# Performance work log

Hardware: AMD Instinct MI355X
Metric: run time of the kernel (lower is better)

## Reference

```python
import jax, jax.numpy as jnp
import numpy as np

POS_THR = 0.7
NEG_THR = 0.3
SAMPLE_BATCH = 256
POS_FRAC = 0.5
B, K, H, W, G = 8, 9, 64, 64, 128
A = K * H * W  # 36864 total anchors


def _make_boxes(key, lead_shape, img=1024.0, wmin=16.0, wmax=256.0):
    k1, k2 = jax.random.split(key)
    ctr = jax.random.uniform(k1, lead_shape + (2,), minval=0.0, maxval=img)
    wh = jax.random.uniform(k2, lead_shape + (2,), minval=wmin, maxval=wmax)
    return jnp.concatenate([ctr - wh / 2, ctr + wh / 2], axis=-1)


def setup_inputs() -> dict:
    key = jax.random.key(0)
    k1, k2, k3, k4 = jax.random.split(key, 4)
    return {
        "cls_logits": jax.random.normal(k1, (B, K, H, W), dtype=jnp.float32),
        "bbox_pred": jax.random.normal(k2, (B, 4 * K, H, W), dtype=jnp.float32) * 0.1,
        "anchors": _make_boxes(k3, (A,)),
        "gt_boxes": _make_boxes(k4, (B, G)),
    }


def _compute_iou(a, g):
    # a: [A,4], g: [G,4] -> [A,G]
    lt = jnp.maximum(a[:, None, :2], g[None, :, :2])
    rb = jnp.minimum(a[:, None, 2:], g[None, :, 2:])
    wh = jnp.clip(rb - lt, 0.0)
    inter = wh[..., 0] * wh[..., 1]
    area_a = (a[:, 2] - a[:, 0]) * (a[:, 3] - a[:, 1])
    area_g = (g[:, 2] - g[:, 0]) * (g[:, 3] - g[:, 1])
    return inter / (area_a[:, None] + area_g[None, :] - inter + 1e-6)


def _encode(anchors, gt):
    aw = anchors[:, 2] - anchors[:, 0]
    ah = anchors[:, 3] - anchors[:, 1]
    acx = (anchors[:, 0] + anchors[:, 2]) / 2
    acy = (anchors[:, 1] + anchors[:, 3]) / 2
    gw = gt[:, 2] - gt[:, 0]
    gh = gt[:, 3] - gt[:, 1]
    gcx = (gt[:, 0] + gt[:, 2]) / 2
    gcy = (gt[:, 1] + gt[:, 3]) / 2
    return jnp.stack([(gcx - acx) / aw, (gcy - acy) / ah,
                      jnp.log(gw / aw), jnp.log(gh / ah)], axis=1)


def _subsample(labels, mask, target, key):
    # deterministic-key analog of torch.randperm subsampling: random priorities,
    # keep the `target` highest-priority anchors of the masked class.
    score = jnp.where(mask, jax.random.uniform(key, labels.shape), -1.0)
    order = jnp.argsort(-score)
    rank = jnp.zeros_like(order).at[order].set(jnp.arange(order.shape[0]))
    keep = mask & (rank < target)
    return jnp.where(mask & ~keep, -1, labels)


def _per_image(cls_i, box_i, anchors, gt, key):
    iou = _compute_iou(anchors, gt)                      # [A,G]
    max_iou = iou.max(axis=1)
    matched_gt_idx = iou.argmax(axis=1)
    labels = jnp.where(max_iou < NEG_THR, 0, -1)
    labels = jnp.where(max_iou >= POS_THR, 1, labels)
    matched_anchor_idx = iou.argmax(axis=0)              # [G]
    labels = labels.at[matched_anchor_idx].set(1)        # force best anchor per gt
    bbox_targets = _encode(anchors, gt[matched_gt_idx])  # [A,4]

    k1, k2 = jax.random.split(key)
    pos_mask0 = labels == 1
    num_pos = pos_mask0.sum()
    target_pos = jnp.minimum(jnp.int32(SAMPLE_BATCH * POS_FRAC), num_pos)
    labels = _subsample(labels, pos_mask0, target_pos, k1)
    neg_mask0 = labels == 0
    num_neg = neg_mask0.sum()
    target_neg = jnp.minimum(SAMPLE_BATCH - target_pos, num_neg)
    labels = _subsample(labels, neg_mask0, target_neg, k2)

    valid = (labels >= 0).astype(cls_i.dtype)
    z = (labels == 1).astype(cls_i.dtype)
    # BCEWithLogits: softplus(x) - x*z
    bce = jax.nn.softplus(cls_i) - cls_i * z
    cls_loss = (bce * valid).sum() / jnp.maximum(valid.sum(), 1.0)

    pos = (labels == 1).astype(cls_i.dtype)
    d = box_i - bbox_targets
    ad = jnp.abs(d)
    sl1 = jnp.where(ad < 1.0, 0.5 * d * d, ad - 0.5)     # SmoothL1, beta=1
    bbox_loss = (sl1 * pos[:, None]).sum() / jnp.maximum(4.0 * pos.sum(), 1.0)
    return cls_loss, bbox_loss


def reference(cls_logits, bbox_pred, anchors, gt_boxes):
    b = cls_logits.shape[0]
    cls = cls_logits.transpose(0, 2, 3, 1).reshape(b, -1)          # [B,A]
    box = bbox_pred.transpose(0, 2, 3, 1).reshape(b, -1, 4)        # [B,A,4]
    keys = jax.random.split(jax.random.key(42), b)
    cls_l, box_l = jax.vmap(_per_image, in_axes=(0, 0, None, 0, 0))(
        cls, box, anchors, gt_boxes, keys)
    cls_loss = cls_l.mean()
    bbox_loss = box_l.mean()
    return jnp.stack([cls_loss, bbox_loss, cls_loss + bbox_loss])
```

## Files before the change

### kernel.cpp

```cpp
#include <hip/hip_runtime.h>
#include <stdint.h>
#include <limits.h>

#define PARTITIONABLE 1

#define B_ 8
#define K_ 9
#define H_ 64
#define W_ 64
#define G_ 128
#define A_ 36864
#define HALF_A 18432
#define NBUCK 1024
#define BSHIFT 13
#define CAP 1024
#define NLAB  1152
#define NPB   144

struct KeyParams { uint32_t k[B_][4]; };

__host__ __device__ static inline uint32_t rotl32(uint32_t x, int r) {
  return (x << r) | (x >> (32 - r));
}

__host__ __device__ static inline void tf2x32(uint32_t k0, uint32_t k1,
                                              uint32_t x0, uint32_t x1,
                                              uint32_t& o0, uint32_t& o1) {
  uint32_t ks2 = k0 ^ k1 ^ 0x1BD11BDAu;
  x0 += k0; x1 += k1;
#define TF_R(r) { x0 += x1; x1 = rotl32(x1, r); x1 ^= x0; }
  TF_R(13) TF_R(15) TF_R(26) TF_R(6)
  x0 += k1;  x1 += ks2 + 1u;
  TF_R(17) TF_R(29) TF_R(16) TF_R(24)
  x0 += ks2; x1 += k0 + 2u;
  TF_R(13) TF_R(15) TF_R(26) TF_R(6)
  x0 += k0;  x1 += k1 + 3u;
  TF_R(17) TF_R(29) TF_R(16) TF_R(24)
  x0 += k1;  x1 += ks2 + 4u;
  TF_R(13) TF_R(15) TF_R(26) TF_R(6)
  x0 += ks2; x1 += k0 + 5u;
#undef TF_R
  o0 = x0; o1 = x1;
}

__device__ static inline uint32_t anchor_vbits(uint32_t k0, uint32_t k1, int a) {
  uint32_t o0, o1;
#if PARTITIONABLE
  tf2x32(k0, k1, 0u, (uint32_t)a, o0, o1);
  return (o0 ^ o1) >> 9;
#else
  if (a < HALF_A) { tf2x32(k0, k1, (uint32_t)a, (uint32_t)(a + HALF_A), o0, o1); return o0 >> 9; }
  else            { tf2x32(k0, k1, (uint32_t)(a - HALF_A), (uint32_t)a, o0, o1); return o1 >> 9; }
#endif
}

__device__ static inline float area_of(float x0, float y0, float x1, float y1) {
#pragma clang fp contract(off)
  return (x1 - x0) * (y1 - y0);
}

__device__ static inline float iou_pre_a(float a0, float a1, float a2, float a3,
                                         float area_a,
                                         float g0, float g1, float g2, float g3) {
#pragma clang fp contract(off)
  float ltx = fmaxf(a0, g0), lty = fmaxf(a1, g1);
  float rbx = fminf(a2, g2), rby = fminf(a3, g3);
  float w = rbx - ltx; w = (w < 0.f) ? 0.f : w;
  float h = rby - lty; h = (h < 0.f) ? 0.f : h;
  float inter  = w * h;
  float area_g = (g2 - g0) * (g3 - g1);
  return inter / (area_a + area_g - inter + 1e-6f);
}

__device__ static inline void encode4(float4 an, float4 gg, float* tt) {
#pragma clang fp contract(off)
  float aw  = an.z - an.x,            ah  = an.w - an.y;
  float acx = (an.x + an.z) * 0.5f,   acy = (an.y + an.w) * 0.5f;
  float gw  = gg.z - gg.x,            gh  = gg.w - gg.y;
  float gcx = (gg.x + gg.z) * 0.5f,   gcy = (gg.y + gg.w) * 0.5f;
  tt[0] = (gcx - acx) / aw;
  tt[1] = (gcy - acy) / ah;
  tt[2] = logf(gw / aw);
  tt[3] = logf(gh / ah);
}

__device__ static inline int block_reduce_int(int v, int* sh) {
  int t = threadIdx.x;
  sh[t] = v; __syncthreads();
  for (int s = 128; s > 0; s >>= 1) { if (t < s) sh[t] += sh[t + s]; __syncthreads(); }
  int r = sh[0]; __syncthreads();
  return r;
}
__device__ static inline float block_reduce_float(float v, float* sh) {
  int t = threadIdx.x;
  sh[t] = v; __syncthreads();
  for (int s = 128; s > 0; s >>= 1) { if (t < s) sh[t] += sh[t + s]; __syncthreads(); }
  float r = sh[0]; __syncthreads();
  return r;
}

__device__ static inline void st_agent_i32(int* p, int v) {
  __hip_atomic_store(p, v, __ATOMIC_RELAXED, __HIP_MEMORY_SCOPE_AGENT);
}
__device__ static inline void st_agent_u32(uint32_t* p, uint32_t v) {
  __hip_atomic_store(p, v, __ATOMIC_RELAXED, __HIP_MEMORY_SCOPE_AGENT);
}
__device__ static inline int ld_agent_i32(const int* p) {
  return __hip_atomic_load(p, __ATOMIC_RELAXED, __HIP_MEMORY_SCOPE_AGENT);
}
__device__ static inline uint32_t ld_agent_u32(const uint32_t* p) {
  return __hip_atomic_load(p, __ATOMIC_RELAXED, __HIP_MEMORY_SCOPE_AGENT);
}
__device__ static inline unsigned long long ld_agent_u64(const unsigned long long* p) {
  return __hip_atomic_load(p, __ATOMIC_RELAXED, __HIP_MEMORY_SCOPE_AGENT);
}
__device__ static inline float ld_agent_f32(const float* p) {
  return __hip_atomic_load(p, __ATOMIC_RELAXED, __HIP_MEMORY_SCOPE_AGENT);
}

__global__ __launch_bounds__(256) void iou_k(
    const float* __restrict__ anchors, const float* __restrict__ gtb,
    int* __restrict__ labels, int* __restrict__ mgt,
    uint32_t* __restrict__ vpos, uint32_t* __restrict__ vneg,
    int* __restrict__ ghist, int* __restrict__ counts,
    unsigned long long* __restrict__ gmax,
    int* __restrict__ cbR, int* __restrict__ targets,
    int* __restrict__ tickets, KeyParams kp) {
  __shared__ float2 gp01[2 * G_];
  __shared__ float2 gp23[2 * G_];
  __shared__ unsigned long long slot2[2 * G_];
  __shared__ int red[256];
  __shared__ int sup[16];
  __shared__ int last;

  const int bid = blockIdx.x;
  const int t = threadIdx.x;
  const int b  = bid / NPB;
  const int xb = bid % NPB;
  const int a  = xb * 256 + t;
  const size_t idx = (size_t)b * A_ + a;

  {
    if (t < G_) {
      float4 gg = ((const float4*)gtb)[b * G_ + t];
      float2 p01; p01.x = gg.x; p01.y = gg.y;
      float2 p23; p23.x = gg.z; p23.y = gg.w;
      gp01[t] = p01; gp01[t + G_] = p01;
      gp23[t] = p23; gp23[t + G_] = p23;
    }
    slot2[t] = 0ull;
    __syncthreads();

    float4 an = ((const float4*)anchors)[a];
    float area_a = area_of(an.x, an.y, an.z, an.w);
    const int t7 = t & (G_ - 1);
    const unsigned long long alow = (unsigned long long)(~(uint32_t)a);
    unsigned long long blp = 0ull;
#pragma unroll 4
    for (int s = 0; s < G_; s++) {
      const int gi = t7 + s;
      float2 p01 = gp01[gi];
      float2 p23 = gp23[gi];
      float v = iou_pre_a(an.x, an.y, an.z, an.w, area_a,
                          p01.x, p01.y, p23.x, p23.y);
      unsigned long long hi = (unsigned long long)__float_as_uint(v) << 32;
      unsigned long long lp = hi | (unsigned)((gi & (G_ - 1)) ^ (G_ - 1));
      if (lp > blp) blp = lp;
      atomicMax(&slot2[gi], hi | alow);
    }
    __syncthreads();
    if (t < G_) {
      unsigned long long p = slot2[t];
      unsigned long long q = slot2[t + G_];
      if (q > p) p = q;
      atomicMax(&gmax[b * G_ + t], p);
    }

    float bv = __uint_as_float((uint32_t)(blp >> 32));
    int   bi = ((int)(blp & (unsigned long long)(G_ - 1))) ^ (G_ - 1);
    int lb = (bv < 0.3f) ? 0 : ((bv >= 0.7f) ? 1 : -1);
    uint32_t vp = anchor_vbits(kp.k[b][0], kp.k[b][1], a);
    uint32_t vn = anchor_vbits(kp.k[b][2], kp.k[b][3], a);
    st_agent_i32(&labels[idx], lb);
    st_agent_u32(&vpos[idx], vp);
    st_agent_u32(&vneg[idx], vn);
    mgt[idx] = bi;
    if (lb == 1)      atomicAdd(&ghist[(b * 2 + 0) * NBUCK + (vp >> BSHIFT)], 1);
    else if (lb == 0) atomicAdd(&ghist[(b * 2 + 1) * NBUCK + (vn >> BSHIFT)], 1);
    int packed = (lb == 1 ? 1 : 0) | ((lb == 0 ? 1 : 0) << 16);
    int rr = block_reduce_int(packed, red);
    if (t == 0) {
      atomicAdd(&counts[b * 2 + 0], rr & 0xFFFF);
      atomicAdd(&counts[b * 2 + 1], rr >> 16);
    }
  }

  __syncthreads();
  if (t == 0) {
    int v = __hip_atomic_fetch_add(&tickets[b], 1, __ATOMIC_RELAXED,
                                   __HIP_MEMORY_SCOPE_AGENT);
    last = (v == NPB - 1);
  }
  __syncthreads();
  if (!last) return;

  if (t < G_) {
    unsigned long long gm = ld_agent_u64(&gmax[b * G_ + t]);
    int fa = (int)(~(uint32_t)(gm & 0xFFFFFFFFull));
    size_t fidx = (size_t)b * A_ + fa;
    int old = atomicExch(&labels[fidx], 1);
    if (old != 1) {
      atomicAdd(&counts[b * 2 + 0], 1);
      atomicAdd(&ghist[(b * 2 + 0) * NBUCK + (ld_agent_u32(&vpos[fidx]) >> BSHIFT)], 1);
      if (old == 0) {
        atomicSub(&counts[b * 2 + 1], 1);
        atomicSub(&ghist[(b * 2 + 1) * NBUCK + (ld_agent_u32(&vneg[fidx]) >> BSHIFT)], 1);
      }
    }
  }
  __syncthreads();

  int npos = ld_agent_i32(&counts[b * 2 + 0]);
  int nneg = ld_agent_i32(&counts[b * 2 + 1]);
  int tp = npos < 128 ? npos : 128;
  int tn = 256 - tp; if (nneg < tn) tn = nneg;
  for (int c = 0; c < 2; ++c) {
    const int row = b * 2 + c;
    const int target = (c == 0) ? tp : tn;
    const int* hist = ghist + (size_t)row * NBUCK;
    { int s = 0; const int base = t * 4;
      for (int i = 0; i < 4; i++) s += ld_agent_i32(&hist[base + i]);
      red[t] = s; }
    __syncthreads();
    if (t < 16) { int ss = 0; for (int j = 0; j < 16; j++) ss += red[t * 16 + j]; sup[t] = ss; }
    __syncthreads();
    if (t == 0) {
      int cb = INT_MAX, R = 0;
      if (target > 0) {
        int cum = 0, si = 0;
        for (int i = 15; i >= 0; i--) { if (cum + sup[i] >= target) { si = i; break; } cum += sup[i]; }
        int sj = si * 16;
        for (int j = si * 16 + 15; j >= si * 16; j--) { if (cum + red[j] >= target) { sj = j; break; } cum += red[j]; }
        for (int k = sj * 4 + 3; k >= sj * 4; k--) {
          int hv = ld_agent_i32(&hist[k]);
          if (cum + hv >= target) { cb = k; R = target - cum; break; }
          cum += hv;
        }
      }
      st_agent_i32(&cbR[row * 2 + 0], cb);
      st_agent_i32(&cbR[row * 2 + 1], R);
      st_agent_i32(&targets[row], target);
    }
    __syncthreads();
  }
}

__global__ __launch_bounds__(256) void loss2_k(
    const float* __restrict__ anchors, const float* __restrict__ gtb,
    const float* __restrict__ cls, const float* __restrict__ boxp,
    const int* __restrict__ labels, const int* __restrict__ mgt,
    const uint32_t* __restrict__ vpos, const uint32_t* __restrict__ vneg,
    const int* __restrict__ cbR, const int* __restrict__ targets,
    int* __restrict__ ccnt, uint32_t* __restrict__ cvv, int* __restrict__ cii,
    float* __restrict__ bsums, int* __restrict__ tickets,
    float* __restrict__ out) {
  __shared__ float redf[256];
  __shared__ uint32_t scv[CAP];
  __shared__ int sci[CAP];
  __shared__ int last;

  const int bid = blockIdx.x;
  const int t = threadIdx.x;
  const int b  = bid / NPB;
  const int xb = bid % NPB;
  const int a  = xb * 256 + t;
  const size_t idx = (size_t)b * A_ + a;

  {
    float sb = 0.f, ss = 0.f;
    int lb = labels[idx];
    if (lb >= 0) {
      int c = (lb == 1) ? 0 : 1;
      int row = b * 2 + c;
      uint32_t v = (c == 0 ? vpos : vneg)[idx];
      int bucket = (int)(v >> BSHIFT);
      int cb = cbR[row * 2];
      if (bucket == cb) {
        int p = atomicAdd(&ccnt[row], 1);
        if (p < CAP) {
          st_agent_u32(&cvv[row * CAP + p], v);
          st_agent_i32(&cii[row * CAP + p], a);
        }
      } else if (bucket > cb) {
        int kk = a % K_; int hw = a / K_; int hh = hw / W_; int wx = hw % W_;
        float x  = cls[(((size_t)b * K_ + kk) * H_ + hh) * W_ + wx];
        float sp = fmaxf(x, 0.f) + log1pf(expf(-fabsf(x)));
        sb = (lb == 1) ? (sp - x) : sp;
        if (lb == 1) {
          float4 an = ((const float4*)anchors)[a];
          int    mg = mgt[idx];
          float4 gg = ((const float4*)gtb)[b * G_ + mg];
          float tt[4]; encode4(an, gg, tt);
          for (int cc2 = 0; cc2 < 4; cc2++) {
            float p = boxp[(((size_t)b * (4 * K_) + (4 * kk + cc2)) * H_ + hh) * W_ + wx];
            float d = p - tt[cc2];
            float ad = fabsf(d);
            ss += (ad < 1.f) ? (0.5f * d * d) : (ad - 0.5f);
          }
        }
      }
    }
    float sbT = block_reduce_float(sb, redf);
    float ssT = block_reduce_float(ss, redf);
    if (t == 0) {
      if (sbT != 0.f) atomicAdd(&bsums[b * 2 + 0], sbT);
      if (ssT != 0.f) atomicAdd(&bsums[b * 2 + 1], ssT);
    }
  }

  __syncthreads();
  if (t == 0) {
    int v = __hip_atomic_fetch_add(&tickets[8 + b], 1, __ATOMIC_RELAXED,
                                   __HIP_MEMORY_SCOPE_AGENT);
    last = (v == NPB - 1);
  }
  __syncthreads();
  if (!last) return;

  for (int c = 0; c < 2; ++c) {
    const int row = b * 2 + c;
    int c2 = ld_agent_i32(&ccnt[row]); if (c2 > CAP) c2 = CAP;
    const int R = cbR[row * 2 + 1];
    for (int j = t; j < c2; j += 256) {
      scv[j] = ld_agent_u32(&cvv[row * CAP + j]);
      sci[j] = ld_agent_i32(&cii[row * CAP + j]);
    }
    __syncthreads();
    const bool pos = (c == 0);
    float sbl = 0.f, ssl = 0.f;
    for (int j = t; j < c2; j += 256) {
      uint32_t v = scv[j]; int a2 = sci[j];
      int r = 0;
      for (int k2 = 0; k2 < c2; k2++) {
        uint32_t vk = scv[k2]; int ik = sci[k2];
        if (vk > v || (vk == v && ik < a2)) r++;
      }
      if (r < R) {
        int kk = a2 % K_; int hw = a2 / K_; int hh = hw / W_; int wx = hw % W_;
        float x = cls[(((size_t)b * K_ + kk) * H_ + hh) * W_ + wx];
        float sp = fmaxf(x, 0.f) + log1pf(expf(-fabsf(x)));
        sbl += pos ? (sp - x) : sp;
        if (pos) {
          float4 an = ((const float4*)anchors)[a2];
          int mg = mgt[(size_t)b * A_ + a2];
          float4 gg = ((const float4*)gtb)[b * G_ + mg];
          float tt[4]; encode4(an, gg, tt);
          for (int cc2 = 0; cc2 < 4; cc2++) {
            float p = boxp[(((size_t)b * (4 * K_) + (4 * kk + cc2)) * H_ + hh) * W_ + wx];
            float d = p - tt[cc2];
            float ad = fabsf(d);
            ssl += (ad < 1.f) ? (0.5f * d * d) : (ad - 0.5f);
          }
        }
      }
    }
    float sbT = block_reduce_float(sbl, redf);
    float ssT = block_reduce_float(ssl, redf);
    if (t == 0) {
      if (sbT != 0.f) atomicAdd(&bsums[b * 2 + 0], sbT);
      if (ssT != 0.f) atomicAdd(&bsums[b * 2 + 1], ssT);
    }
    __syncthreads();
  }

  __syncthreads();
  if (t == 0) {
    int v = __hip_atomic_fetch_add(&tickets[16], 1, __ATOMIC_RELAXED,
                                   __HIP_MEMORY_SCOPE_AGENT);
    last = (v == B_ - 1);
  }
  __syncthreads();
  if (!last) return;

  if (t == 0) {
    float cl = 0.f, bl = 0.f;
    for (int bb = 0; bb < B_; bb++) {
      int tpv = ld_agent_i32(&targets[bb * 2 + 0]);
      int tnv = ld_agent_i32(&targets[bb * 2 + 1]);
      float s0 = ld_agent_f32(&bsums[bb * 2 + 0]);
      float s1 = ld_agent_f32(&bsums[bb * 2 + 1]);
      cl += s0 / fmaxf((float)(tpv + tnv), 1.f);
      bl += s1 / fmaxf(4.f * (float)tpv, 1.f);
    }
    cl *= 0.125f; bl *= 0.125f;
    out[0] = cl; out[1] = bl; out[2] = cl + bl;
  }
}

static void compute_keys(KeyParams& kp) {
  const uint32_t r0 = 0u, r1 = 42u;
#if PARTITIONABLE
  for (int b = 0; b < B_; b++) {
    uint32_t kb0, kb1;
    tf2x32(r0, r1, 0u, (uint32_t)b, kb0, kb1);
    uint32_t a0, a1, c0, c1;
    tf2x32(kb0, kb1, 0u, 0u, a0, a1);
    tf2x32(kb0, kb1, 0u, 1u, c0, c1);
    kp.k[b][0] = a0; kp.k[b][1] = a1; kp.k[b][2] = c0; kp.k[b][3] = c1;
  }
#else
  uint32_t o0[8], o1[8], flat[16];
  for (int i = 0; i < 8; i++) tf2x32(r0, r1, (uint32_t)i, (uint32_t)(8 + i), o0[i], o1[i]);
  for (int i = 0; i < 8; i++) { flat[i] = o0[i]; flat[8 + i] = o1[i]; }
  for (int b = 0; b < B_; b++) {
    uint32_t kb0 = flat[2 * b], kb1 = flat[2 * b + 1];
    uint32_t a0, b0, a1, b1;
    tf2x32(kb0, kb1, 0u, 2u, a0, b0);
    tf2x32(kb0, kb1, 1u, 3u, a1, b1);
    kp.k[b][0] = a0; kp.k[b][1] = a1; kp.k[b][2] = b0; kp.k[b][3] = b1;
  }
#endif
}

extern "C" void kernel_launch(void* const* d_in, const int* in_sizes, int n_in,
                              void* d_out, int out_size, void* d_ws, size_t ws_size,
                              hipStream_t stream) {
  const float* cls     = (const float*)d_in[0];
  const float* boxp    = (const float*)d_in[1];
  const float* anchors = (const float*)d_in[2];
  const float* gtb     = (const float*)d_in[3];
  float* out = (float*)d_out;

  uint8_t* w = (uint8_t*)d_ws;
  unsigned long long* gmax = (unsigned long long*)w;
  int*      ghist   = (int*)(w + 8192);
  int*      counts  = (int*)(w + 73728);
  int*      ccnt    = (int*)(w + 73856);
  float*    bsums   = (float*)(w + 73984);
  int*      tickets = (int*)(w + 74112);
  int*      labels  = (int*)(w + 74240);
  int*      mgt     = labels + (size_t)B_ * A_;
  uint32_t* vpos    = (uint32_t*)(mgt + (size_t)B_ * A_);
  uint32_t* vneg    = vpos + (size_t)B_ * A_;
  int*      cbR     = (int*)(vneg + (size_t)B_ * A_);
  int*      targets = cbR + 32;
  uint32_t* cvv     = (uint32_t*)(targets + 16);
  int*      cii     = (int*)(cvv + 16 * CAP);

  KeyParams kp;
  compute_keys(kp);

  (void)hipMemsetAsync(w, 0, 74240, stream);
  iou_k<<<NLAB, 256, 0, stream>>>(anchors, gtb, labels, mgt, vpos, vneg,
                                  ghist, counts, gmax, cbR, targets, tickets, kp);
  loss2_k<<<NLAB, 256, 0, stream>>>(anchors, gtb, cls, boxp, labels, mgt,
                                    vpos, vneg, cbR, targets, ccnt, cvv, cii,
                                    bsums, tickets, out);
}
```

Before: 145.1 us.

## Fuse labeling and loss kernels; per-image last block does sampling and loss

Merges the IoU/label kernel and the loss kernel into one launch. The last block of each image scans all 36864 labels, collects kept and boundary-bucket candidates into shared memory, ranks the boundary candidates, and computes the loss over at most 256 kept anchors. This removes the second kernel launch, its full-grid pass, and the global candidate buffers. It also precomputes gt areas in shared memory and replaces the IoU division with a hardware reciprocal plus one Newton step, which may differ slightly from exact division. The trade-off is a serial per-image tail in a single block and fixed shared-memory caps on the kept and candidate lists.

Result: slower. 208.1 us (+43.4%).

```diff
diff --git a/kernel.cpp b/kernel.cpp
--- a/kernel.cpp
+++ b/kernel.cpp
@@ -3,6 +3,7 @@
 #include <limits.h>
 
 #define PARTITIONABLE 1
+#define EXACT_DIV 0
 
 #define B_ 8
 #define K_ 9
@@ -13,7 +14,8 @@
 #define HALF_A 18432
 #define NBUCK 1024
 #define BSHIFT 13
-#define CAP 1024
+#define CCAP 256
+#define KCAP 320
 #define NLAB  1152
 #define NPB   144
 
@@ -59,19 +61,6 @@
   return (x1 - x0) * (y1 - y0);
 }
 
-__device__ static inline float iou_pre_a(float a0, float a1, float a2, float a3,
-                                         float area_a,
-                                         float g0, float g1, float g2, float g3) {
-#pragma clang fp contract(off)
-  float ltx = fmaxf(a0, g0), lty = fmaxf(a1, g1);
-  float rbx = fminf(a2, g2), rby = fminf(a3, g3);
-  float w = rbx - ltx; w = (w < 0.f) ? 0.f : w;
-  float h = rby - lty; h = (h < 0.f) ? 0.f : h;
-  float inter  = w * h;
-  float area_g = (g2 - g0) * (g3 - g1);
-  return inter / (area_a + area_g - inter + 1e-6f);
-}
-
 __device__ static inline void encode4(float4 an, float4 gg, float* tt) {
 #pragma clang fp contract(off)
   float aw  = an.z - an.x,            ah  = an.w - an.y;
@@ -118,20 +107,27 @@
   return __hip_atomic_load(p, __ATOMIC_RELAXED, __HIP_MEMORY_SCOPE_AGENT);
 }
 
-__global__ __launch_bounds__(256) void iou_k(
+__global__ __launch_bounds__(256) void mega2_k(
     const float* __restrict__ anchors, const float* __restrict__ gtb,
+    const float* __restrict__ cls, const float* __restrict__ boxp,
     int* __restrict__ labels, int* __restrict__ mgt,
     uint32_t* __restrict__ vpos, uint32_t* __restrict__ vneg,
     int* __restrict__ ghist, int* __restrict__ counts,
     unsigned long long* __restrict__ gmax,
-    int* __restrict__ cbR, int* __restrict__ targets,
-    int* __restrict__ tickets, KeyParams kp) {
-  __shared__ float2 gp01[2 * G_];
-  __shared__ float2 gp23[2 * G_];
+    int* __restrict__ targets, float* __restrict__ bsums,
+    int* __restrict__ tickets, float* __restrict__ out, KeyParams kp) {
+  __shared__ float4 gbox[2 * G_];
+  __shared__ float  garea[2 * G_];
   __shared__ unsigned long long slot2[2 * G_];
   __shared__ int red[256];
   __shared__ int sup[16];
   __shared__ int last;
+  __shared__ int tcb[2], tR[2], ttp[2];
+  __shared__ int nkeep, ncand[2];
+  __shared__ uint32_t cv[2][CCAP];
+  __shared__ int      ca[2][CCAP];
+  __shared__ int      keepA[KCAP];
+  __shared__ float redf[256];
 
   const int bid = blockIdx.x;
   const int t = threadIdx.x;
@@ -143,10 +139,9 @@
   {
     if (t < G_) {
       float4 gg = ((const float4*)gtb)[b * G_ + t];
-      float2 p01; p01.x = gg.x; p01.y = gg.y;
-      float2 p23; p23.x = gg.z; p23.y = gg.w;
-      gp01[t] = p01; gp01[t + G_] = p01;
-      gp23[t] = p23; gp23[t + G_] = p23;
+      gbox[t] = gg; gbox[t + G_] = gg;
+      float ag = area_of(gg.x, gg.y, gg.z, gg.w);
+      garea[t] = ag; garea[t + G_] = ag;
     }
     slot2[t] = 0ull;
     __syncthreads();
@@ -159,11 +154,26 @@
 #pragma unroll 4
     for (int s = 0; s < G_; s++) {
       const int gi = t7 + s;
-      float2 p01 = gp01[gi];
-      float2 p23 = gp23[gi];
-      float v = iou_pre_a(an.x, an.y, an.z, an.w, area_a,
-                          p01.x, p01.y, p23.x, p23.y);
-      unsigned long long hi = (unsigned long long)__float_as_uint(v) << 32;
+      float4 gg = gbox[gi];
+      float ag  = garea[gi];
+      float q;
+      {
+#pragma clang fp contract(off)
+        float ltx = fmaxf(an.x, gg.x), lty = fmaxf(an.y, gg.y);
+        float rbx = fminf(an.z, gg.z), rby = fminf(an.w, gg.w);
+        float w = rbx - ltx; w = (w < 0.f) ? 0.f : w;
+        float h = rby - lty; h = (h < 0.f) ? 0.f : h;
+        float inter = w * h;
+        float denom = area_a + ag - inter + 1e-6f;
+#if EXACT_DIV
+        q = inter / denom;
+#else
+        float r0 = __builtin_amdgcn_rcpf(denom);
+        float r1 = r0 * __builtin_fmaf(-denom, r0, 2.0f);
+        q = inter * r1;
+#endif
+      }
+      unsigned long long hi = (unsigned long long)__float_as_uint(q) << 32;
       unsigned long long lp = hi | (unsigned)((gi & (G_ - 1)) ^ (G_ - 1));
       if (lp > blp) blp = lp;
       atomicMax(&slot2[gi], hi | alow);
@@ -171,8 +181,8 @@
     __syncthreads();
     if (t < G_) {
       unsigned long long p = slot2[t];
-      unsigned long long q = slot2[t + G_];
-      if (q > p) p = q;
+      unsigned long long q2 = slot2[t + G_];
+      if (q2 > p) p = q2;
       atomicMax(&gmax[b * G_ + t], p);
     }
 
@@ -184,7 +194,7 @@
     st_agent_i32(&labels[idx], lb);
     st_agent_u32(&vpos[idx], vp);
     st_agent_u32(&vneg[idx], vn);
-    mgt[idx] = bi;
+    st_agent_i32(&mgt[idx], bi);
     if (lb == 1)      atomicAdd(&ghist[(b * 2 + 0) * NBUCK + (vp >> BSHIFT)], 1);
     else if (lb == 0) atomicAdd(&ghist[(b * 2 + 1) * NBUCK + (vn >> BSHIFT)], 1);
     int packed = (lb == 1 ? 1 : 0) | ((lb == 0 ? 1 : 0) << 16);
@@ -200,6 +210,7 @@
     int v = __hip_atomic_fetch_add(&tickets[b], 1, __ATOMIC_RELAXED,
                                    __HIP_MEMORY_SCOPE_AGENT);
     last = (v == NPB - 1);
+    nkeep = 0; ncand[0] = 0; ncand[1] = 0;
   }
   __syncthreads();
   if (!last) return;
@@ -220,93 +231,100 @@
   }
   __syncthreads();
 
-  int npos = ld_agent_i32(&counts[b * 2 + 0]);
-  int nneg = ld_agent_i32(&counts[b * 2 + 1]);
-  int tp = npos < 128 ? npos : 128;
-  int tn = 256 - tp; if (nneg < tn) tn = nneg;
-  for (int c = 0; c < 2; ++c) {
-    const int row = b * 2 + c;
-    const int target = (c == 0) ? tp : tn;
-    const int* hist = ghist + (size_t)row * NBUCK;
-    { int s = 0; const int base = t * 4;
-      for (int i = 0; i < 4; i++) s += ld_agent_i32(&hist[base + i]);
-      red[t] = s; }
+  {
+    int npos = ld_agent_i32(&counts[b * 2 + 0]);
+    int nneg = ld_agent_i32(&counts[b * 2 + 1]);
+    int tp = npos < 128 ? npos : 128;
+    int tn = 256 - tp; if (nneg < tn) tn = nneg;
+    for (int c = 0; c < 2; ++c) {
+      const int row = b * 2 + c;
+      const int target = (c == 0) ? tp : tn;
+      const int* hist = ghist + (size_t)row * NBUCK;
+      { int s = 0; const int base = t * 4;
+        for (int i = 0; i < 4; i++) s += ld_agent_i32(&hist[base + i]);
+        red[t] = s; }
+      __syncthreads();
+      if (t < 16) { int ss = 0; for (int j = 0; j < 16; j++) ss += red[t * 16 + j]; sup[t] = ss; }
+      __syncthreads();
+      if (t == 0) {
+        int cb = INT_MAX, R = 0;
+        if (target > 0) {
+          int cum = 0, si = 0;
+          for (int i = 15; i >= 0; i--) { if (cum + sup[i] >= target) { si = i; break; } cum += sup[i]; }
+          int sj = si * 16;
+          for (int j = si * 16 + 15; j >= si * 16; j--) { if (cum + red[j] >= target) { sj = j; break; } cum += red[j]; }
+          for (int k = sj * 4 + 3; k >= sj * 4; k--) {
+            int hv = ld_agent_i32(&hist[k]);
+            if (cum + hv >= target) { cb = k; R = target - cum; break; }
+            cum += hv;
+          }
+        }
+        tcb[c] = cb; tR[c] = R; ttp[c] = target;
+        st_agent_i32(&targets[row], target);
+      }
+      __syncthreads();
+    }
+  }
+
+  {
+    const int cb0 = tcb[0], cb1 = tcb[1];
+    for (int i = t; i < A_; i += 256) {
+      size_t ii = (size_t)b * A_ + i;
+      int lb = ld_agent_i32(&labels[ii]);
+      if (lb < 0) continue;
+      int c = (lb == 1) ? 0 : 1;
+      uint32_t v = ld_agent_u32(c == 0 ? &vpos[ii] : &vneg[ii]);
+      int bk = (int)(v >> BSHIFT);
+      int cb = (c == 0) ? cb0 : cb1;
+      if (bk > cb) {
+        int p = atomicAdd(&nkeep, 1);
+        if (p < KCAP) keepA[p] = i | (c << 16);
+      } else if (bk == cb) {
+        int p = atomicAdd(&ncand[c], 1);
+        if (p < CCAP) { cv[c][p] = v; ca[c][p] = i; }
+      }
+    }
     __syncthreads();
-    if (t < 16) { int ss = 0; for (int j = 0; j < 16; j++) ss += red[t * 16 + j]; sup[t] = ss; }
+    for (int c = 0; c < 2; ++c) {
+      int n = ncand[c]; if (n > CCAP) n = CCAP;
+      const int R = tR[c];
+      for (int j = t; j < n; j += 256) {
+        uint32_t v = cv[c][j]; int a2 = ca[c][j];
+        int r = 0;
+        for (int k2 = 0; k2 < n; k2++) {
+          uint32_t vk = cv[c][k2];
+          if (vk > v || (vk == v && ca[c][k2] < a2)) r++;
+        }
+        if (r < R) {
+          int p = atomicAdd(&nkeep, 1);
+          if (p < KCAP) keepA[p] = a2 | (c << 16);
+        }
+      }
+    }
     __syncthreads();
-    if (t == 0) {
-      int cb = INT_MAX, R = 0;
-      if (target > 0) {
-        int cum = 0, si = 0;
-        for (int i = 15; i >= 0; i--) { if (cum + sup[i] >= target) { si = i; break; } cum += sup[i]; }
-        int sj = si * 16;
-        for (int j = si * 16 + 15; j >= si * 16; j--) { if (cum + red[j] >= target) { sj = j; break; } cum += red[j]; }
-        for (int k = sj * 4 + 3; k >= sj * 4; k--) {
-          int hv = ld_agent_i32(&hist[k]);
-          if (cum + hv >= target) { cb = k; R = target - cum; break; }
-          cum += hv;
-        }
-      }
-      st_agent_i32(&cbR[row * 2 + 0], cb);
-      st_agent_i32(&cbR[row * 2 + 1], R);
-      st_agent_i32(&targets[row], target);
-    }
-    __syncthreads();
-  }
-}
-
-__global__ __launch_bounds__(256) void loss2_k(
-    const float* __restrict__ anchors, const float* __restrict__ gtb,
-    const float* __restrict__ cls, const float* __restrict__ boxp,
-    const int* __restrict__ labels, const int* __restrict__ mgt,
-    const uint32_t* __restrict__ vpos, const uint32_t* __restrict__ vneg,
-    const int* __restrict__ cbR, const int* __restrict__ targets,
-    int* __restrict__ ccnt, uint32_t* __restrict__ cvv, int* __restrict__ cii,
-    float* __restrict__ bsums, int* __restrict__ tickets,
-    float* __restrict__ out) {
-  __shared__ float redf[256];
-  __shared__ uint32_t scv[CAP];
-  __shared__ int sci[CAP];
-  __shared__ int last;
-
-  const int bid = blockIdx.x;
-  const int t = threadIdx.x;
-  const int b  = bid / NPB;
-  const int xb = bid % NPB;
-  const int a  = xb * 256 + t;
-  const size_t idx = (size_t)b * A_ + a;
+  }
 
   {
+    int nk = nkeep; if (nk > KCAP) nk = KCAP;
     float sb = 0.f, ss = 0.f;
-    int lb = labels[idx];
-    if (lb >= 0) {
-      int c = (lb == 1) ? 0 : 1;
-      int row = b * 2 + c;
-      uint32_t v = (c == 0 ? vpos : vneg)[idx];
-      int bucket = (int)(v >> BSHIFT);
-      int cb = cbR[row * 2];
-      if (bucket == cb) {
-        int p = atomicAdd(&ccnt[row], 1);
-        if (p < CAP) {
-          st_agent_u32(&cvv[row * CAP + p], v);
-          st_agent_i32(&cii[row * CAP + p], a);
-        }
-      } else if (bucket > cb) {
-        int kk = a % K_; int hw = a / K_; int hh = hw / W_; int wx = hw % W_;
-        float x  = cls[(((size_t)b * K_ + kk) * H_ + hh) * W_ + wx];
-        float sp = fmaxf(x, 0.f) + log1pf(expf(-fabsf(x)));
-        sb = (lb == 1) ? (sp - x) : sp;
-        if (lb == 1) {
-          float4 an = ((const float4*)anchors)[a];
-          int    mg = mgt[idx];
-          float4 gg = ((const float4*)gtb)[b * G_ + mg];
-          float tt[4]; encode4(an, gg, tt);
-          for (int cc2 = 0; cc2 < 4; cc2++) {
-            float p = boxp[(((size_t)b * (4 * K_) + (4 * kk + cc2)) * H_ + hh) * W_ + wx];
-            float d = p - tt[cc2];
-            float ad = fabsf(d);
-            ss += (ad < 1.f) ? (0.5f * d * d) : (ad - 0.5f);
-          }
+    for (int j = t; j < nk; j += 256) {
+      int e = keepA[j];
+      int a2 = e & 0xFFFF;
+      bool pos = ((e >> 16) == 0);
+      int kk = a2 % K_; int hw = a2 / K_; int hh = hw / W_; int wx = hw % W_;
+      float x = cls[(((size_t)b * K_ + kk) * H_ + hh) * W_ + wx];
+      float sp = fmaxf(x, 0.f) + log1pf(expf(-fabsf(x)));
+      sb += pos ? (sp - x) : sp;
+      if (pos) {
+        float4 an = ((const float4*)anchors)[a2];
+        int mg = ld_agent_i32(&mgt[(size_t)b * A_ + a2]);
+        float4 gg = ((const float4*)gtb)[b * G_ + mg];
+        float tt[4]; encode4(an, gg, tt);
+        for (int cc2 = 0; cc2 < 4; cc2++) {
+          float p = boxp[(((size_t)b * (4 * K_) + (4 * kk + cc2)) * H_ + hh) * W_ + wx];
+          float d = p - tt[cc2];
+          float ad = fabsf(d);
+          ss += (ad < 1.f) ? (0.5f * d * d) : (ad - 0.5f);
         }
       }
     }
@@ -320,62 +338,7 @@
 
   __syncthreads();
   if (t == 0) {
-    int v = __hip_atomic_fetch_add(&tickets[8 + b], 1, __ATOMIC_RELAXED,
-                                   __HIP_MEMORY_SCOPE_AGENT);
-    last = (v == NPB - 1);
-  }
-  __syncthreads();
-  if (!last) return;
-
-  for (int c = 0; c < 2; ++c) {
-    const int row = b * 2 + c;
-    int c2 = ld_agent_i32(&ccnt[row]); if (c2 > CAP) c2 = CAP;
-    const int R = cbR[row * 2 + 1];
-    for (int j = t; j < c2; j += 256) {
-      scv[j] = ld_agent_u32(&cvv[row * CAP + j]);
-      sci[j] = ld_agent_i32(&cii[row * CAP + j]);
-    }
-    __syncthreads();
-    const bool pos = (c == 0);
-    float sbl = 0.f, ssl = 0.f;
-    for (int j = t; j < c2; j += 256) {
-      uint32_t v = scv[j]; int a2 = sci[j];
-      int r = 0;
-      for (int k2 = 0; k2 < c2; k2++) {
-        uint32_t vk = scv[k2]; int ik = sci[k2];
-        if (vk > v || (vk == v && ik < a2)) r++;
-      }
-      if (r < R) {
-        int kk = a2 % K_; int hw = a2 / K_; int hh = hw / W_; int wx = hw % W_;
-        float x = cls[(((size_t)b * K_ + kk) * H_ + hh) * W_ + wx];
-        float sp = fmaxf(x, 0.f) + log1pf(expf(-fabsf(x)));
-        sbl += pos ? (sp - x) : sp;
-        if (pos) {
-          float4 an = ((const float4*)anchors)[a2];
-          int mg = mgt[(size_t)b * A_ + a2];
-          float4 gg = ((const float4*)gtb)[b * G_ + mg];
-          float tt[4]; encode4(an, gg, tt);
-          for (int cc2 = 0; cc2 < 4; cc2++) {
-            float p = boxp[(((size_t)b * (4 * K_) + (4 * kk + cc2)) * H_ + hh) * W_ + wx];
-            float d = p - tt[cc2];
-            float ad = fabsf(d);
-            ssl += (ad < 1.f) ? (0.5f * d * d) : (ad - 0.5f);
-          }
-        }
-      }
-    }
-    float sbT = block_reduce_float(sbl, redf);
-    float ssT = block_reduce_float(ssl, redf);
-    if (t == 0) {
-      if (sbT != 0.f) atomicAdd(&bsums[b * 2 + 0], sbT);
-      if (ssT != 0.f) atomicAdd(&bsums[b * 2 + 1], ssT);
-    }
-    __syncthreads();
-  }
-
-  __syncthreads();
-  if (t == 0) {
-    int v = __hip_atomic_fetch_add(&tickets[16], 1, __ATOMIC_RELAXED,
+    int v = __hip_atomic_fetch_add(&tickets[B_], 1, __ATOMIC_RELAXED,
                                    __HIP_MEMORY_SCOPE_AGENT);
     last = (v == B_ - 1);
   }
@@ -435,25 +398,19 @@
   unsigned long long* gmax = (unsigned long long*)w;
   int*      ghist   = (int*)(w + 8192);
   int*      counts  = (int*)(w + 73728);
-  int*      ccnt    = (int*)(w + 73856);
-  float*    bsums   = (float*)(w + 73984);
-  int*      tickets = (int*)(w + 74112);
+  float*    bsums   = (float*)(w + 73856);
+  int*      tickets = (int*)(w + 73984);
   int*      labels  = (int*)(w + 74240);
   int*      mgt     = labels + (size_t)B_ * A_;
   uint32_t* vpos    = (uint32_t*)(mgt + (size_t)B_ * A_);
   uint32_t* vneg    = vpos + (size_t)B_ * A_;
-  int*      cbR     = (int*)(vneg + (size_t)B_ * A_);
-  int*      targets = cbR + 32;
-  uint32_t* cvv     = (uint32_t*)(targets + 16);
-  int*      cii     = (int*)(cvv + 16 * CAP);
+  int*      targets = (int*)(vneg + (size_t)B_ * A_);
 
   KeyParams kp;
   compute_keys(kp);
 
   (void)hipMemsetAsync(w, 0, 74240, stream);
-  iou_k<<<NLAB, 256, 0, stream>>>(anchors, gtb, labels, mgt, vpos, vneg,
-                                  ghist, counts, gmax, cbR, targets, tickets, kp);
-  loss2_k<<<NLAB, 256, 0, stream>>>(anchors, gtb, cls, boxp, labels, mgt,
-                                    vpos, vneg, cbR, targets, ccnt, cvv, cii,
-                                    bsums, tickets, out);
-}
+  mega2_k<<<NLAB, 256, 0, stream>>>(anchors, gtb, cls, boxp, labels, mgt,
+                                    vpos, vneg, ghist, counts, gmax,
+                                    targets, bsums, tickets, out, kp);
+}
```

## Pack per-anchor state into one u64 and trim IoU inner loop

Applied to the files above, without the earlier changes.

Replaces the four per-anchor arrays (label, matched gt, pos and neg random bits) with a single packed 64-bit word, and computes only the random stream needed for each anchor's label. Forced positives are marked with a high bit through atomicOr. The IoU loop now uses precomputed gt areas and float4 shared loads, with a hardware reciprocal plus one Newton step in place of the division. Block count reductions become wavefront ballots, and the candidate buffer cap shrinks from 1024 to 256. The reciprocal may differ from IEEE division in the last bit, which can flip exact threshold or tie comparisons, and the smaller cap could overflow if a bucket holds many anchors.

Measured after the change: 191.7 us. +32.2%, slower.

```diff
diff --git a/kernel.cpp b/kernel.cpp
--- a/kernel.cpp
+++ b/kernel.cpp
@@ -13,7 +13,8 @@
 #define HALF_A 18432
 #define NBUCK 1024
 #define BSHIFT 13
-#define CAP 1024
+#define VMASK 0x7FFFFFu
+#define CCAP 256
 #define NLAB  1152
 #define NPB   144
 
@@ -59,19 +60,6 @@
   return (x1 - x0) * (y1 - y0);
 }
 
-__device__ static inline float iou_pre_a(float a0, float a1, float a2, float a3,
-                                         float area_a,
-                                         float g0, float g1, float g2, float g3) {
-#pragma clang fp contract(off)
-  float ltx = fmaxf(a0, g0), lty = fmaxf(a1, g1);
-  float rbx = fminf(a2, g2), rby = fminf(a3, g3);
-  float w = rbx - ltx; w = (w < 0.f) ? 0.f : w;
-  float h = rby - lty; h = (h < 0.f) ? 0.f : h;
-  float inter  = w * h;
-  float area_g = (g2 - g0) * (g3 - g1);
-  return inter / (area_a + area_g - inter + 1e-6f);
-}
-
 __device__ static inline void encode4(float4 an, float4 gg, float* tt) {
 #pragma clang fp contract(off)
   float aw  = an.z - an.x,            ah  = an.w - an.y;
@@ -84,13 +72,6 @@
   tt[3] = logf(gh / ah);
 }
 
-__device__ static inline int block_reduce_int(int v, int* sh) {
-  int t = threadIdx.x;
-  sh[t] = v; __syncthreads();
-  for (int s = 128; s > 0; s >>= 1) { if (t < s) sh[t] += sh[t + s]; __syncthreads(); }
-  int r = sh[0]; __syncthreads();
-  return r;
-}
 __device__ static inline float block_reduce_float(float v, float* sh) {
   int t = threadIdx.x;
   sh[t] = v; __syncthreads();
@@ -99,6 +80,9 @@
   return r;
 }
 
+__device__ static inline void st_agent_u64(unsigned long long* p, unsigned long long v) {
+  __hip_atomic_store(p, v, __ATOMIC_RELAXED, __HIP_MEMORY_SCOPE_AGENT);
+}
 __device__ static inline void st_agent_i32(int* p, int v) {
   __hip_atomic_store(p, v, __ATOMIC_RELAXED, __HIP_MEMORY_SCOPE_AGENT);
 }
@@ -120,14 +104,13 @@
 
 __global__ __launch_bounds__(256) void iou_k(
     const float* __restrict__ anchors, const float* __restrict__ gtb,
-    int* __restrict__ labels, int* __restrict__ mgt,
-    uint32_t* __restrict__ vpos, uint32_t* __restrict__ vneg,
+    unsigned long long* __restrict__ pk,
     int* __restrict__ ghist, int* __restrict__ counts,
     unsigned long long* __restrict__ gmax,
     int* __restrict__ cbR, int* __restrict__ targets,
     int* __restrict__ tickets, KeyParams kp) {
-  __shared__ float2 gp01[2 * G_];
-  __shared__ float2 gp23[2 * G_];
+  __shared__ float4 gbox[2 * G_];
+  __shared__ float  garea[2 * G_];
   __shared__ unsigned long long slot2[2 * G_];
   __shared__ int red[256];
   __shared__ int sup[16];
@@ -143,10 +126,9 @@
   {
     if (t < G_) {
       float4 gg = ((const float4*)gtb)[b * G_ + t];
-      float2 p01; p01.x = gg.x; p01.y = gg.y;
-      float2 p23; p23.x = gg.z; p23.y = gg.w;
-      gp01[t] = p01; gp01[t + G_] = p01;
-      gp23[t] = p23; gp23[t + G_] = p23;
+      gbox[t] = gg; gbox[t + G_] = gg;
+      float ag = area_of(gg.x, gg.y, gg.z, gg.w);
+      garea[t] = ag; garea[t + G_] = ag;
     }
     slot2[t] = 0ull;
     __syncthreads();
@@ -159,11 +141,22 @@
 #pragma unroll 4
     for (int s = 0; s < G_; s++) {
       const int gi = t7 + s;
-      float2 p01 = gp01[gi];
-      float2 p23 = gp23[gi];
-      float v = iou_pre_a(an.x, an.y, an.z, an.w, area_a,
-                          p01.x, p01.y, p23.x, p23.y);
-      unsigned long long hi = (unsigned long long)__float_as_uint(v) << 32;
+      float4 gg = gbox[gi];
+      float ag  = garea[gi];
+      float q;
+      {
+#pragma clang fp contract(off)
+        float ltx = fmaxf(an.x, gg.x), lty = fmaxf(an.y, gg.y);
+        float rbx = fminf(an.z, gg.z), rby = fminf(an.w, gg.w);
+        float w = rbx - ltx; w = (w < 0.f) ? 0.f : w;
+        float h = rby - lty; h = (h < 0.f) ? 0.f : h;
+        float inter = w * h;
+        float denom = area_a + ag - inter + 1e-6f;
+        float r0 = __builtin_amdgcn_rcpf(denom);
+        float r1 = r0 * __builtin_fmaf(-denom, r0, 2.0f);
+        q = inter * r1;
+      }
+      unsigned long long hi = (unsigned long long)__float_as_uint(q) << 32;
       unsigned long long lp = hi | (unsigned)((gi & (G_ - 1)) ^ (G_ - 1));
       if (lp > blp) blp = lp;
       atomicMax(&slot2[gi], hi | alow);
@@ -171,27 +164,28 @@
     __syncthreads();
     if (t < G_) {
       unsigned long long p = slot2[t];
-      unsigned long long q = slot2[t + G_];
-      if (q > p) p = q;
+      unsigned long long q2 = slot2[t + G_];
+      if (q2 > p) p = q2;
       atomicMax(&gmax[b * G_ + t], p);
     }
 
     float bv = __uint_as_float((uint32_t)(blp >> 32));
     int   bi = ((int)(blp & (unsigned long long)(G_ - 1))) ^ (G_ - 1);
     int lb = (bv < 0.3f) ? 0 : ((bv >= 0.7f) ? 1 : -1);
-    uint32_t vp = anchor_vbits(kp.k[b][0], kp.k[b][1], a);
-    uint32_t vn = anchor_vbits(kp.k[b][2], kp.k[b][3], a);
-    st_agent_i32(&labels[idx], lb);
-    st_agent_u32(&vpos[idx], vp);
-    st_agent_u32(&vneg[idx], vn);
-    mgt[idx] = bi;
-    if (lb == 1)      atomicAdd(&ghist[(b * 2 + 0) * NBUCK + (vp >> BSHIFT)], 1);
-    else if (lb == 0) atomicAdd(&ghist[(b * 2 + 1) * NBUCK + (vn >> BSHIFT)], 1);
-    int packed = (lb == 1 ? 1 : 0) | ((lb == 0 ? 1 : 0) << 16);
-    int rr = block_reduce_int(packed, red);
-    if (t == 0) {
-      atomicAdd(&counts[b * 2 + 0], rr & 0xFFFF);
-      atomicAdd(&counts[b * 2 + 1], rr >> 16);
+    uint32_t kk0 = (lb == 0) ? kp.k[b][2] : kp.k[b][0];
+    uint32_t kk1 = (lb == 0) ? kp.k[b][3] : kp.k[b][1];
+    uint32_t vv = anchor_vbits(kk0, kk1, a);
+    unsigned long long pack = (unsigned long long)vv
+                            | ((unsigned long long)(uint32_t)bi << 23)
+                            | ((unsigned long long)(uint32_t)(lb + 1) << 30);
+    st_agent_u64(&pk[idx], pack);
+    if (lb == 1)      atomicAdd(&ghist[(b * 2 + 0) * NBUCK + (vv >> BSHIFT)], 1);
+    else if (lb == 0) atomicAdd(&ghist[(b * 2 + 1) * NBUCK + (vv >> BSHIFT)], 1);
+    unsigned long long mpos = __ballot(lb == 1);
+    unsigned long long mneg = __ballot(lb == 0);
+    if ((t & 63) == 0) {
+      if (mpos) atomicAdd(&counts[b * 2 + 0], __popcll(mpos));
+      if (mneg) atomicAdd(&counts[b * 2 + 1], __popcll(mneg));
     }
   }
 
@@ -208,65 +202,73 @@
     unsigned long long gm = ld_agent_u64(&gmax[b * G_ + t]);
     int fa = (int)(~(uint32_t)(gm & 0xFFFFFFFFull));
     size_t fidx = (size_t)b * A_ + fa;
-    int old = atomicExch(&labels[fidx], 1);
-    if (old != 1) {
-      atomicAdd(&counts[b * 2 + 0], 1);
-      atomicAdd(&ghist[(b * 2 + 0) * NBUCK + (ld_agent_u32(&vpos[fidx]) >> BSHIFT)], 1);
-      if (old == 0) {
-        atomicSub(&counts[b * 2 + 1], 1);
-        atomicSub(&ghist[(b * 2 + 1) * NBUCK + (ld_agent_u32(&vneg[fidx]) >> BSHIFT)], 1);
-      }
-    }
-  }
-  __syncthreads();
-
-  int npos = ld_agent_i32(&counts[b * 2 + 0]);
-  int nneg = ld_agent_i32(&counts[b * 2 + 1]);
-  int tp = npos < 128 ? npos : 128;
-  int tn = 256 - tp; if (nneg < tn) tn = nneg;
-  for (int c = 0; c < 2; ++c) {
-    const int row = b * 2 + c;
-    const int target = (c == 0) ? tp : tn;
-    const int* hist = ghist + (size_t)row * NBUCK;
-    { int s = 0; const int base = t * 4;
-      for (int i = 0; i < 4; i++) s += ld_agent_i32(&hist[base + i]);
-      red[t] = s; }
-    __syncthreads();
-    if (t < 16) { int ss = 0; for (int j = 0; j < 16; j++) ss += red[t * 16 + j]; sup[t] = ss; }
-    __syncthreads();
-    if (t == 0) {
-      int cb = INT_MAX, R = 0;
-      if (target > 0) {
-        int cum = 0, si = 0;
-        for (int i = 15; i >= 0; i--) { if (cum + sup[i] >= target) { si = i; break; } cum += sup[i]; }
-        int sj = si * 16;
-        for (int j = si * 16 + 15; j >= si * 16; j--) { if (cum + red[j] >= target) { sj = j; break; } cum += red[j]; }
-        for (int k = sj * 4 + 3; k >= sj * 4; k--) {
-          int hv = ld_agent_i32(&hist[k]);
-          if (cum + hv >= target) { cb = k; R = target - cum; break; }
-          cum += hv;
+    unsigned long long old = atomicOr(&pk[fidx], 1ull << 63);
+    if (!(old >> 63)) {
+      int oldlb = (int)((old >> 30) & 3) - 1;
+      if (oldlb != 1) {
+        atomicAdd(&counts[b * 2 + 0], 1);
+        uint32_t vpf = (oldlb == -1) ? (uint32_t)(old & VMASK)
+                                     : anchor_vbits(kp.k[b][0], kp.k[b][1], fa);
+        atomicAdd(&ghist[(b * 2 + 0) * NBUCK + (vpf >> BSHIFT)], 1);
+        if (oldlb == 0) {
+          atomicSub(&counts[b * 2 + 1], 1);
+          atomicSub(&ghist[(b * 2 + 1) * NBUCK + ((uint32_t)(old & VMASK) >> BSHIFT)], 1);
+          st_agent_u64(&pk[fidx], (old & ~(unsigned long long)VMASK)
+                                  | vpf | (1ull << 63));
         }
       }
-      st_agent_i32(&cbR[row * 2 + 0], cb);
-      st_agent_i32(&cbR[row * 2 + 1], R);
-      st_agent_i32(&targets[row], target);
-    }
-    __syncthreads();
+    }
+  }
+  __syncthreads();
+
+  {
+    int npos = ld_agent_i32(&counts[b * 2 + 0]);
+    int nneg = ld_agent_i32(&counts[b * 2 + 1]);
+    int tp = npos < 128 ? npos : 128;
+    int tn = 256 - tp; if (nneg < tn) tn = nneg;
+    for (int c = 0; c < 2; ++c) {
+      const int row = b * 2 + c;
+      const int target = (c == 0) ? tp : tn;
+      const int* hist = ghist + (size_t)row * NBUCK;
+      { int s = 0; const int base = t * 4;
+        for (int i = 0; i < 4; i++) s += ld_agent_i32(&hist[base + i]);
+        red[t] = s; }
+      __syncthreads();
+      if (t < 16) { int ss = 0; for (int j = 0; j < 16; j++) ss += red[t * 16 + j]; sup[t] = ss; }
+      __syncthreads();
+      if (t == 0) {
+        int cb = INT_MAX, R = 0;
+        if (target > 0) {
+          int cum = 0, si = 0;
+          for (int i = 15; i >= 0; i--) { if (cum + sup[i] >= target) { si = i; break; } cum += sup[i]; }
+          int sj = si * 16;
+          for (int j = si * 16 + 15; j >= si * 16; j--) { if (cum + red[j] >= target) { sj = j; break; } cum += red[j]; }
+          for (int k = sj * 4 + 3; k >= sj * 4; k--) {
+            int hv = ld_agent_i32(&hist[k]);
+            if (cum + hv >= target) { cb = k; R = target - cum; break; }
+            cum += hv;
+          }
+        }
+        st_agent_i32(&cbR[row * 2 + 0], cb);
+        st_agent_i32(&cbR[row * 2 + 1], R);
+        st_agent_i32(&targets[row], target);
+      }
+      __syncthreads();
+    }
   }
 }
 
 __global__ __launch_bounds__(256) void loss2_k(
     const float* __restrict__ anchors, const float* __restrict__ gtb,
     const float* __restrict__ cls, const float* __restrict__ boxp,
-    const int* __restrict__ labels, const int* __restrict__ mgt,
-    const uint32_t* __restrict__ vpos, const uint32_t* __restrict__ vneg,
+    const unsigned long long* __restrict__ pk,
     const int* __restrict__ cbR, const int* __restrict__ targets,
     int* __restrict__ ccnt, uint32_t* __restrict__ cvv, int* __restrict__ cii,
     float* __restrict__ bsums, int* __restrict__ tickets,
     float* __restrict__ out) {
   __shared__ float redf[256];
-  __shared__ uint32_t scv[CAP];
-  __shared__ int sci[CAP];
+  __shared__ uint32_t scv[CCAP];
+  __shared__ int sci[CCAP];
   __shared__ int last;
 
   const int bid = blockIdx.x;
@@ -278,32 +280,36 @@
 
   {
     float sb = 0.f, ss = 0.f;
-    int lb = labels[idx];
-    if (lb >= 0) {
-      int c = (lb == 1) ? 0 : 1;
+    unsigned long long p = pk[idx];
+    int lb = (int)((p >> 30) & 3) - 1;
+    bool forced = (p >> 63) != 0;
+    bool pos = forced || (lb == 1);
+    bool neg = !pos && (lb == 0);
+    if (pos || neg) {
+      int c = pos ? 0 : 1;
       int row = b * 2 + c;
-      uint32_t v = (c == 0 ? vpos : vneg)[idx];
+      uint32_t v = (uint32_t)(p & VMASK);
       int bucket = (int)(v >> BSHIFT);
       int cb = cbR[row * 2];
       if (bucket == cb) {
-        int p = atomicAdd(&ccnt[row], 1);
-        if (p < CAP) {
-          st_agent_u32(&cvv[row * CAP + p], v);
-          st_agent_i32(&cii[row * CAP + p], a);
+        int pp = atomicAdd(&ccnt[row], 1);
+        if (pp < CCAP) {
+          st_agent_u32(&cvv[row * CCAP + pp], v);
+          st_agent_i32(&cii[row * CCAP + pp], a);
         }
       } else if (bucket > cb) {
         int kk = a % K_; int hw = a / K_; int hh = hw / W_; int wx = hw % W_;
         float x  = cls[(((size_t)b * K_ + kk) * H_ + hh) * W_ + wx];
         float sp = fmaxf(x, 0.f) + log1pf(expf(-fabsf(x)));
-        sb = (lb == 1) ? (sp - x) : sp;
-        if (lb == 1) {
+        sb = pos ? (sp - x) : sp;
+        if (pos) {
           float4 an = ((const float4*)anchors)[a];
-          int    mg = mgt[idx];
+          int    mg = (int)((p >> 23) & 127);
           float4 gg = ((const float4*)gtb)[b * G_ + mg];
           float tt[4]; encode4(an, gg, tt);
           for (int cc2 = 0; cc2 < 4; cc2++) {
-            float p = boxp[(((size_t)b * (4 * K_) + (4 * kk + cc2)) * H_ + hh) * W_ + wx];
-            float d = p - tt[cc2];
+            float bp = boxp[(((size_t)b * (4 * K_) + (4 * kk + cc2)) * H_ + hh) * W_ + wx];
+            float d = bp - tt[cc2];
             float ad = fabsf(d);
             ss += (ad < 1.f) ? (0.5f * d * d) : (ad - 0.5f);
           }
@@ -329,11 +335,11 @@
 
   for (int c = 0; c < 2; ++c) {
     const int row = b * 2 + c;
-    int c2 = ld_agent_i32(&ccnt[row]); if (c2 > CAP) c2 = CAP;
+    int c2 = ld_agent_i32(&ccnt[row]); if (c2 > CCAP) c2 = CCAP;
     const int R = cbR[row * 2 + 1];
     for (int j = t; j < c2; j += 256) {
-      scv[j] = ld_agent_u32(&cvv[row * CAP + j]);
-      sci[j] = ld_agent_i32(&cii[row * CAP + j]);
+      scv[j] = ld_agent_u32(&cvv[row * CCAP + j]);
+      sci[j] = ld_agent_i32(&cii[row * CCAP + j]);
     }
     __syncthreads();
     const bool pos = (c == 0);
@@ -352,12 +358,12 @@
         sbl += pos ? (sp - x) : sp;
         if (pos) {
           float4 an = ((const float4*)anchors)[a2];
-          int mg = mgt[(size_t)b * A_ + a2];
+          int mg = (int)((pk[(size_t)b * A_ + a2] >> 23) & 127);
           float4 gg = ((const float4*)gtb)[b * G_ + mg];
           float tt[4]; encode4(an, gg, tt);
           for (int cc2 = 0; cc2 < 4; cc2++) {
-            float p = boxp[(((size_t)b * (4 * K_) + (4 * kk + cc2)) * H_ + hh) * W_ + wx];
-            float d = p - tt[cc2];
+            float bp = boxp[(((size_t)b * (4 * K_) + (4 * kk + cc2)) * H_ + hh) * W_ + wx];
+            float d = bp - tt[cc2];
             float ad = fabsf(d);
             ssl += (ad < 1.f) ? (0.5f * d * d) : (ad - 0.5f);
           }
@@ -438,22 +444,19 @@
   int*      ccnt    = (int*)(w + 73856);
   float*    bsums   = (float*)(w + 73984);
   int*      tickets = (int*)(w + 74112);
-  int*      labels  = (int*)(w + 74240);
-  int*      mgt     = labels + (size_t)B_ * A_;
-  uint32_t* vpos    = (uint32_t*)(mgt + (size_t)B_ * A_);
-  uint32_t* vneg    = vpos + (size_t)B_ * A_;
-  int*      cbR     = (int*)(vneg + (size_t)B_ * A_);
+  unsigned long long* pkb = (unsigned long long*)(w + 74496);
+  int*      cbR     = (int*)(pkb + (size_t)B_ * A_);
   int*      targets = cbR + 32;
   uint32_t* cvv     = (uint32_t*)(targets + 16);
-  int*      cii     = (int*)(cvv + 16 * CAP);
+  int*      cii     = (int*)(cvv + 16 * CCAP);
 
   KeyParams kp;
   compute_keys(kp);
 
-  (void)hipMemsetAsync(w, 0, 74240, stream);
-  iou_k<<<NLAB, 256, 0, stream>>>(anchors, gtb, labels, mgt, vpos, vneg,
-                                  ghist, counts, gmax, cbR, targets, tickets, kp);
-  loss2_k<<<NLAB, 256, 0, stream>>>(anchors, gtb, cls, boxp, labels, mgt,
-                                    vpos, vneg, cbR, targets, ccnt, cvv, cii,
+  (void)hipMemsetAsync(w, 0, 74496, stream);
+  iou_k<<<NLAB, 256, 0, stream>>>(anchors, gtb, pkb, ghist, counts, gmax,
+                                  cbR, targets, tickets, kp);
+  loss2_k<<<NLAB, 256, 0, stream>>>(anchors, gtb, cls, boxp, pkb,
+                                    cbR, targets, ccnt, cvv, cii,
                                     bsums, tickets, out);
 }
```
